# Kernel tuning notes

Hardware: AMD Instinct MI355X
Metric: run time of the kernel (lower is better)

Reference implementation:

```python
import jax, jax.numpy as jnp
import numpy as np
from jax import lax

N, B, C = 8192, 4, 16
H1, H2 = 64, 128
R = 0.7
K = 64  # max_num_neighbors


def setup_inputs() -> dict:
    key = jax.random.key(0)
    k1, k2, k3, k4, k5, k6 = jax.random.split(key, 6)
    x = jax.random.normal(k1, (N, C), dtype=jnp.float32)
    pos = jax.random.normal(k2, (N, 3), dtype=jnp.float32)
    batch = jnp.repeat(jnp.arange(B, dtype=jnp.int32), N // B)  # sorted segment ids
    # PointConv local MLP: Lin(C+3 -> H1), ReLU, Lin(H1 -> H2), ReLU
    W1 = jax.random.normal(k3, (C + 3, H1), dtype=jnp.float32) * np.sqrt(2.0 / (C + 3)).astype(np.float32)
    b1 = jnp.zeros((H1,), dtype=jnp.float32)
    W2 = jax.random.normal(k4, (H1, H2), dtype=jnp.float32) * np.sqrt(2.0 / H1).astype(np.float32)
    b2 = jnp.zeros((H2,), dtype=jnp.float32)
    return {"x": x, "pos": pos, "batch": batch, "W1": W1, "b1": b1, "W2": W2, "b2": b2}


def reference(x, pos, batch, W1, b1, W2, b2):
    # radius ball query: for every point (idx = arange(N), so all points are
    # centroids) take up to K neighbors within radius R in the same cloud.
    sq = jnp.sum(pos * pos, axis=-1)                       # [N]
    d2 = sq[:, None] + sq[None, :] - 2.0 * (pos @ pos.T)   # [N, N] squared dists
    valid = (d2 <= R * R) & (batch[:, None] == batch[None, :])
    score = jnp.where(valid, -d2, -jnp.inf)
    vals, idx = lax.top_k(score, K)                        # K nearest within ball
    mask = vals > -jnp.inf                                 # [N, K] real-neighbor mask

    # PointConv message: MLP(concat(x_j, pos_j - pos_i)), then max-aggregate.
    x_j = x[idx]                                           # [N, K, C]
    rel = pos[idx] - pos[:, None, :]                       # [N, K, 3]
    h = jnp.concatenate([x_j, rel], axis=-1)               # [N, K, C+3]
    h = jax.nn.relu(h @ W1 + b1)
    h = jax.nn.relu(h @ W2 + b2)                           # [N, K, H2]
    h = jnp.where(mask[..., None], h, -jnp.inf)
    out = jnp.max(h, axis=1)                               # self edge (d2=0) always valid
    return out, pos, batch
```

## Files before the change

kernel.cpp:

```cpp
#include <hip/hip_runtime.h>
#include <hip/hip_bf16.h>
#include <float.h>
#include <stdint.h>

#define NPTS 8192
#define SEG  2048
#define CF   16
#define HID1 64
#define HID2 128
#define KMAX 64
#define R2   0.49f
#define CAP  384
#define NCH  6

typedef unsigned long long ULL;
typedef short bf16x8 __attribute__((ext_vector_type(8)));
typedef float f32x4  __attribute__((ext_vector_type(4)));

__device__ __forceinline__ uint32_t f2ord(float f) {
    uint32_t u = __float_as_uint(f);
    return (u & 0x80000000u) ? ~u : (u | 0x80000000u);
}

__device__ __forceinline__ short f2bf(float f) {
    __hip_bfloat16 h = __float2bfloat16(f);
    union { __hip_bfloat16 b; short s; } u; u.b = h;
    return u.s;
}

__global__ __launch_bounds__(256) void prep_kernel(
    const float* __restrict__ x, const float* __restrict__ pos,
    const int* __restrict__ batch,
    const float* __restrict__ W1, const float* __restrict__ b1,
    const float* __restrict__ W2,
    float* __restrict__ A, float* __restrict__ C,
    float4* __restrict__ pos4, unsigned short* __restrict__ W2T,
    float* __restrict__ out)
{
    const int t = blockIdx.x * 256 + threadIdx.x;
    const int i = t >> 6, k = t & 63;

    const float px = pos[3 * i + 0], py = pos[3 * i + 1], pz = pos[3 * i + 2];
    float c = __fmul_rn(px, W1[16 * HID1 + k]);
    c = fmaf(py, W1[17 * HID1 + k], c);
    c = fmaf(pz, W1[18 * HID1 + k], c);

    float a = b1[k];
    #pragma unroll
    for (int cc = 0; cc < CF; ++cc)
        a = fmaf(x[i * CF + cc], W1[cc * HID1 + k], a);
    a += c;

    A[t] = a;
    C[t] = c;

    if (t < HID1 * HID2) {
        const int cc = t >> 6, kk = t & 63;
        W2T[t] = (unsigned short)f2bf(W2[kk * HID2 + cc]);
    }

    if (k == 0) {
        const float sq = __fadd_rn(__fadd_rn(__fmul_rn(px, px), __fmul_rn(py, py)),
                                   __fmul_rn(pz, pz));
        pos4[i] = make_float4(px, py, pz, sq);
    }
    if (k < 3) out[NPTS * HID2 + 3 * i + k] = pos[3 * i + k];
    if (k == 3) out[NPTS * HID2 + NPTS * 3 + i] = (float)batch[i];
}

__global__ __launch_bounds__(64, 3) void pointconv_kernel(
    const int* __restrict__ batch,
    const unsigned short* __restrict__ W2T, const float* __restrict__ b2,
    const float* __restrict__ A, const float* __restrict__ C,
    const float4* __restrict__ pos4, float* __restrict__ out)
{
    __shared__ ULL s_key[2][CAP];
    __shared__ int s_nbr[2][KMAX];

    const int l  = threadIdx.x;
    const int i0 = blockIdx.x * 2;

    const float4 cw0 = pos4[i0], cw1 = pos4[i0 + 1];
    const int seg0 = batch[i0] * SEG;
    const ULL lmask = (1ull << l) - 1ull;

    int cnt0 = 0, cnt1 = 0;
    #pragma unroll 4
    for (int it = 0; it < SEG / 64; ++it) {
        const int j = seg0 + it * 64 + l;
        const float4 pj = pos4[j];
        const float dot0 = fmaf(cw0.z, pj.z, fmaf(cw0.y, pj.y, __fmul_rn(cw0.x, pj.x)));
        const float d20  = __fsub_rn(__fadd_rn(cw0.w, pj.w), __fmul_rn(2.0f, dot0));
        const float dot1 = fmaf(cw1.z, pj.z, fmaf(cw1.y, pj.y, __fmul_rn(cw1.x, pj.x)));
        const float d21  = __fsub_rn(__fadd_rn(cw1.w, pj.w), __fmul_rn(2.0f, dot1));
        const bool h0 = (d20 <= R2), h1 = (d21 <= R2);
        const ULL m0 = __ballot(h0), m1 = __ballot(h1);
        if (h0) {
            const int p = cnt0 + __popcll(m0 & lmask);
            if (p < CAP) s_key[0][p] = ((ULL)f2ord(d20) << 32) | (unsigned)j;
        }
        cnt0 += __popcll(m0);
        if (h1) {
            const int p = cnt1 + __popcll(m1 & lmask);
            if (p < CAP) s_key[1][p] = ((ULL)f2ord(d21) << 32) | (unsigned)j;
        }
        cnt1 += __popcll(m1);
    }
    if (cnt0 > CAP) cnt0 = CAP;
    if (cnt1 > CAP) cnt1 = CAP;
    const bool nd0 = cnt0 > KMAX, nd1 = cnt1 > KMAX;

    uint32_t eo0[NCH], ej0[NCH], eo1[NCH], ej1[NCH];
    if (!nd0) {
        if (l < KMAX) s_nbr[0][l] = (l < cnt0) ? (int)(s_key[0][l] & 0xffffffffu) : i0;
    } else {
        #pragma unroll
        for (int g = 0; g < NCH; ++g) {
            eo0[g] = 0xffffffffu; ej0[g] = 0xffffffffu;
            if (64 * g < cnt0) {
                const int e = l + 64 * g;
                if (e < cnt0) {
                    const ULL kk = s_key[0][e];
                    eo0[g] = (uint32_t)(kk >> 32);
                    ej0[g] = (uint32_t)(kk & 0xffffffffu);
                }
            }
        }
    }
    if (!nd1) {
        if (l < KMAX) s_nbr[1][l] = (l < cnt1) ? (int)(s_key[1][l] & 0xffffffffu) : i0 + 1;
    } else {
        #pragma unroll
        for (int g = 0; g < NCH; ++g) {
            eo1[g] = 0xffffffffu; ej1[g] = 0xffffffffu;
            if (64 * g < cnt1) {
                const int e = l + 64 * g;
                if (e < cnt1) {
                    const ULL kk = s_key[1][e];
                    eo1[g] = (uint32_t)(kk >> 32);
                    ej1[g] = (uint32_t)(kk & 0xffffffffu);
                }
            }
        }
    }

    if (nd0 || nd1) {
        const uint32_t ORDR2 = 0x80000000u | __float_as_uint(R2);
        uint32_t lo0 = 0u, hi0 = nd0 ? ORDR2 : 0u;
        uint32_t lo1 = 0u, hi1 = nd1 ? ORDR2 : 0u;
        while ((lo0 < hi0) | (lo1 < hi1)) {
            if (lo0 < hi0) {
                const uint32_t mid = lo0 + ((hi0 - lo0) >> 1);
                int c = 0;
                #pragma unroll
                for (int g = 0; g < NCH; ++g)
                    if (64 * g < cnt0) c += __popcll(__ballot(eo0[g] <= mid));
                if (c >= KMAX) hi0 = mid; else lo0 = mid + 1;
            }
            if (lo1 < hi1) {
                const uint32_t mid = lo1 + ((hi1 - lo1) >> 1);
                int c = 0;
                #pragma unroll
                for (int g = 0; g < NCH; ++g)
                    if (64 * g < cnt1) c += __popcll(__ballot(eo1[g] <= mid));
                if (c >= KMAX) hi1 = mid; else lo1 = mid + 1;
            }
        }
        const uint32_t T0 = lo0, T1 = lo1;

        int cLT0 = 0, cLE0 = 0, cLT1 = 0, cLE1 = 0;
        if (nd0) {
            #pragma unroll
            for (int g = 0; g < NCH; ++g) {
                cLT0 += __popcll(__ballot(eo0[g] < T0));
                cLE0 += __popcll(__ballot(eo0[g] <= T0));
            }
        }
        if (nd1) {
            #pragma unroll
            for (int g = 0; g < NCH; ++g) {
                cLT1 += __popcll(__ballot(eo1[g] < T1));
                cLE1 += __popcll(__ballot(eo1[g] <= T1));
            }
        }

        uint32_t J0 = 0xffffffffu, J1 = 0xffffffffu;
        const bool tb0 = nd0 && (cLE0 > KMAX), tb1 = nd1 && (cLE1 > KMAX);
        if (tb0 | tb1) {
            uint32_t jlo0 = 0u, jhi0 = tb0 ? (NPTS - 1) : 0u;
            uint32_t jlo1 = 0u, jhi1 = tb1 ? (NPTS - 1) : 0u;
            const int need0 = KMAX - cLT0, need1 = KMAX - cLT1;
            while ((jlo0 < jhi0) | (jlo1 < jhi1)) {
                if (jlo0 < jhi0) {
                    const uint32_t jmid = jlo0 + ((jhi0 - jlo0) >> 1);
                    int c = 0;
                    #pragma unroll
                    for (int g = 0; g < NCH; ++g)
                        if (64 * g < cnt0) c += __popcll(__ballot(eo0[g] == T0 && ej0[g] <= jmid));
                    if (c >= need0) jhi0 = jmid; else jlo0 = jmid + 1;
                }
                if (jlo1 < jhi1) {
                    const uint32_t jmid = jlo1 + ((jhi1 - jlo1) >> 1);
                    int c = 0;
                    #pragma unroll
                    for (int g = 0; g < NCH; ++g)
                        if (64 * g < cnt1) c += __popcll(__ballot(eo1[g] == T1 && ej1[g] <= jmid));
                    if (c >= need1) jhi1 = jmid; else jlo1 = jmid + 1;
                }
            }
            if (tb0) J0 = jlo0;
            if (tb1) J1 = jlo1;
        }

        if (nd0) {
            int sb = 0;
            #pragma unroll
            for (int g = 0; g < NCH; ++g) {
                if (64 * g < cnt0) {
                    const bool take = (eo0[g] < T0) || ((eo0[g] == T0) && (ej0[g] <= J0));
                    const ULL mk = __ballot(take);
                    if (take) s_nbr[0][sb + __popcll(mk & lmask)] = (int)ej0[g];
                    sb += __popcll(mk);
                }
            }
        }
        if (nd1) {
            int sb = 0;
            #pragma unroll
            for (int g = 0; g < NCH; ++g) {
                if (64 * g < cnt1) {
                    const bool take = (eo1[g] < T1) || ((eo1[g] == T1) && (ej1[g] <= J1));
                    const ULL mk = __ballot(take);
                    if (take) s_nbr[1][sb + __popcll(mk & lmask)] = (int)ej1[g];
                    sb += __popcll(mk);
                }
            }
        }
    }

    const int r = l & 15, q = l >> 4;
    const int mm[2] = { cnt0 < KMAX ? cnt0 : KMAX, cnt1 < KMAX ? cnt1 : KMAX };

    bf16x8 af[2][4][2];
    #pragma unroll
    for (int ci = 0; ci < 2; ++ci) {
        const int iw = i0 + ci;
        float cv[2][8];
        {
            const float4* Cv = (const float4*)(C + (size_t)iw * HID1);
            #pragma unroll
            for (int kc = 0; kc < 2; ++kc) {
                const float4 c0 = Cv[kc * 8 + q * 2], c1 = Cv[kc * 8 + q * 2 + 1];
                cv[kc][0] = c0.x; cv[kc][1] = c0.y; cv[kc][2] = c0.z; cv[kc][3] = c0.w;
                cv[kc][4] = c1.x; cv[kc][5] = c1.y; cv[kc][6] = c1.z; cv[kc][7] = c1.w;
            }
        }
        #pragma unroll
        for (int t = 0; t < 4; ++t) {
            const int row = t * 16 + r;
            const int j = s_nbr[ci][row];
            const float4* Aj = (const float4*)(A + (size_t)j * HID1);
            #pragma unroll
            for (int kc = 0; kc < 2; ++kc) {
                const float4 a0 = Aj[kc * 8 + q * 2], a1 = Aj[kc * 8 + q * 2 + 1];
                bf16x8 v;
                v[0] = f2bf(fmaxf(a0.x - cv[kc][0], 0.0f));
                v[1] = f2bf(fmaxf(a0.y - cv[kc][1], 0.0f));
                v[2] = f2bf(fmaxf(a0.z - cv[kc][2], 0.0f));
                v[3] = f2bf(fmaxf(a0.w - cv[kc][3], 0.0f));
                v[4] = f2bf(fmaxf(a1.x - cv[kc][4], 0.0f));
                v[5] = f2bf(fmaxf(a1.y - cv[kc][5], 0.0f));
                v[6] = f2bf(fmaxf(a1.z - cv[kc][6], 0.0f));
                v[7] = f2bf(fmaxf(a1.w - cv[kc][7], 0.0f));
                af[ci][t][kc] = v;
            }
        }
    }

    #pragma unroll
    for (int cb = 0; cb < 8; ++cb) {
        f32x4 acc[2][4];
        #pragma unroll
        for (int ci = 0; ci < 2; ++ci)
            #pragma unroll
            for (int t = 0; t < 4; ++t) acc[ci][t] = (f32x4){0.f, 0.f, 0.f, 0.f};

        #pragma unroll
        for (int kc = 0; kc < 2; ++kc) {
            const bf16x8 bf =
                *(const bf16x8*)&W2T[(cb * 16 + r) * HID1 + kc * 32 + q * 8];
            #pragma unroll
            for (int ci = 0; ci < 2; ++ci)
                #pragma unroll
                for (int t = 0; t < 4; ++t)
                    acc[ci][t] = __builtin_amdgcn_mfma_f32_16x16x32_bf16(
                        af[ci][t][kc], bf, acc[ci][t], 0, 0, 0);
        }

        const int c = cb * 16 + r;
        #pragma unroll
        for (int ci = 0; ci < 2; ++ci) {
            float v = -FLT_MAX;
            #pragma unroll
            for (int t = 0; t < 4; ++t) {
                const int nb = t * 16 + q * 4;
                #pragma unroll
                for (int reg = 0; reg < 4; ++reg)
                    if (nb + reg < mm[ci]) v = fmaxf(v, acc[ci][t][reg]);
            }
            v = fmaxf(v, __shfl_xor(v, 16));
            v = fmaxf(v, __shfl_xor(v, 32));
            if (q == 0)
                out[(size_t)(i0 + ci) * HID2 + c] = fmaxf(v + b2[c], 0.0f);
        }
    }
}

extern "C" void kernel_launch(void* const* d_in, const int* in_sizes, int n_in,
                              void* d_out, int out_size, void* d_ws, size_t ws_size,
                              hipStream_t stream) {
    const float* x     = (const float*)d_in[0];
    const float* pos   = (const float*)d_in[1];
    const int*   batch = (const int*)d_in[2];
    const float* W1    = (const float*)d_in[3];
    const float* b1    = (const float*)d_in[4];
    const float* W2    = (const float*)d_in[5];
    const float* b2    = (const float*)d_in[6];
    float* out = (float*)d_out;

    float*  A    = (float*)d_ws;
    float*  C    = A + (size_t)NPTS * HID1;
    float4* P4   = (float4*)(C + (size_t)NPTS * HID1);
    unsigned short* W2T = (unsigned short*)(P4 + NPTS);

    hipLaunchKernelGGL(prep_kernel, dim3(NPTS * HID1 / 256), dim3(256), 0, stream,
                       x, pos, batch, W1, b1, W2, A, C, P4, W2T, out);
    hipLaunchKernelGGL(pointconv_kernel, dim3(NPTS / 2), dim3(64), 0, stream,
                       batch, W2T, b2, A, C, P4, out);
}
```

Before: 54.07 us.

## Process four centroids per block and share the neighbor scan across two waves

Each block now has two wavefronts and handles four centroids instead of two. Every neighbor position loaded in the scan is tested against all four centroids, and the segment is split between the two waves, so position traffic per centroid is halved. Candidate compaction now uses shared-memory atomic counters instead of wave ballots and prefix popcounts, which adds a block barrier. Each wave then runs selection and the MFMA stage for its two centroids. LDS atomics contend when many lanes hit the same centroid, and shared memory per block roughly doubles.

```diff
diff --git a/kernel.cpp b/kernel.cpp
--- a/kernel.cpp
+++ b/kernel.cpp
@@ -68,51 +68,57 @@
     if (k == 3) out[NPTS * HID2 + NPTS * 3 + i] = (float)batch[i];
 }
 
-__global__ __launch_bounds__(64, 3) void pointconv_kernel(
+__global__ __launch_bounds__(128, 3) void pointconv_kernel(
     const int* __restrict__ batch,
     const unsigned short* __restrict__ W2T, const float* __restrict__ b2,
     const float* __restrict__ A, const float* __restrict__ C,
     const float4* __restrict__ pos4, float* __restrict__ out)
 {
-    __shared__ ULL s_key[2][CAP];
-    __shared__ int s_nbr[2][KMAX];
-
-    const int l  = threadIdx.x;
-    const int i0 = blockIdx.x * 2;
-
-    const float4 cw0 = pos4[i0], cw1 = pos4[i0 + 1];
+    __shared__ ULL s_key[4][CAP];
+    __shared__ int s_nbr[4][KMAX];
+    __shared__ int s_cnt[4];
+
+    const int tid = threadIdx.x;
+    const int w   = tid >> 6, l = tid & 63;
+    const int i0  = blockIdx.x * 4;
+    const ULL lmask = (1ull << l) - 1ull;
+
+    if (tid < 4) s_cnt[tid] = 0;
+
+    float4 cw[4];
+    #pragma unroll
+    for (int ci = 0; ci < 4; ++ci) cw[ci] = pos4[i0 + ci];
     const int seg0 = batch[i0] * SEG;
-    const ULL lmask = (1ull << l) - 1ull;
-
-    int cnt0 = 0, cnt1 = 0;
-    #pragma unroll 4
-    for (int it = 0; it < SEG / 64; ++it) {
-        const int j = seg0 + it * 64 + l;
+    __syncthreads();
+
+    const int base = seg0 + w * (SEG / 2);
+    #pragma unroll 2
+    for (int it = 0; it < SEG / 128; ++it) {
+        const int j = base + it * 64 + l;
         const float4 pj = pos4[j];
-        const float dot0 = fmaf(cw0.z, pj.z, fmaf(cw0.y, pj.y, __fmul_rn(cw0.x, pj.x)));
-        const float d20  = __fsub_rn(__fadd_rn(cw0.w, pj.w), __fmul_rn(2.0f, dot0));
-        const float dot1 = fmaf(cw1.z, pj.z, fmaf(cw1.y, pj.y, __fmul_rn(cw1.x, pj.x)));
-        const float d21  = __fsub_rn(__fadd_rn(cw1.w, pj.w), __fmul_rn(2.0f, dot1));
-        const bool h0 = (d20 <= R2), h1 = (d21 <= R2);
-        const ULL m0 = __ballot(h0), m1 = __ballot(h1);
-        if (h0) {
-            const int p = cnt0 + __popcll(m0 & lmask);
-            if (p < CAP) s_key[0][p] = ((ULL)f2ord(d20) << 32) | (unsigned)j;
-        }
-        cnt0 += __popcll(m0);
-        if (h1) {
-            const int p = cnt1 + __popcll(m1 & lmask);
-            if (p < CAP) s_key[1][p] = ((ULL)f2ord(d21) << 32) | (unsigned)j;
-        }
-        cnt1 += __popcll(m1);
-    }
+        #pragma unroll
+        for (int ci = 0; ci < 4; ++ci) {
+            const float dot = fmaf(cw[ci].z, pj.z,
+                              fmaf(cw[ci].y, pj.y, __fmul_rn(cw[ci].x, pj.x)));
+            const float d2  = __fsub_rn(__fadd_rn(cw[ci].w, pj.w), __fmul_rn(2.0f, dot));
+            if (d2 <= R2) {
+                const int p = atomicAdd(&s_cnt[ci], 1);
+                if (p < CAP)
+                    s_key[ci][p] = ((ULL)f2ord(d2) << 32) | (unsigned)j;
+            }
+        }
+    }
+    __syncthreads();
+
+    const int c0i = 2 * w, c1i = 2 * w + 1;
+    int cnt0 = s_cnt[c0i], cnt1 = s_cnt[c1i];
     if (cnt0 > CAP) cnt0 = CAP;
     if (cnt1 > CAP) cnt1 = CAP;
     const bool nd0 = cnt0 > KMAX, nd1 = cnt1 > KMAX;
 
     uint32_t eo0[NCH], ej0[NCH], eo1[NCH], ej1[NCH];
     if (!nd0) {
-        if (l < KMAX) s_nbr[0][l] = (l < cnt0) ? (int)(s_key[0][l] & 0xffffffffu) : i0;
+        if (l < KMAX) s_nbr[c0i][l] = (l < cnt0) ? (int)(s_key[c0i][l] & 0xffffffffu) : i0 + c0i;
     } else {
         #pragma unroll
         for (int g = 0; g < NCH; ++g) {
@@ -120,7 +126,7 @@
             if (64 * g < cnt0) {
                 const int e = l + 64 * g;
                 if (e < cnt0) {
-                    const ULL kk = s_key[0][e];
+                    const ULL kk = s_key[c0i][e];
                     eo0[g] = (uint32_t)(kk >> 32);
                     ej0[g] = (uint32_t)(kk & 0xffffffffu);
                 }
@@ -128,7 +134,7 @@
         }
     }
     if (!nd1) {
-        if (l < KMAX) s_nbr[1][l] = (l < cnt1) ? (int)(s_key[1][l] & 0xffffffffu) : i0 + 1;
+        if (l < KMAX) s_nbr[c1i][l] = (l < cnt1) ? (int)(s_key[c1i][l] & 0xffffffffu) : i0 + c1i;
     } else {
         #pragma unroll
         for (int g = 0; g < NCH; ++g) {
@@ -136,7 +142,7 @@
             if (64 * g < cnt1) {
                 const int e = l + 64 * g;
                 if (e < cnt1) {
-                    const ULL kk = s_key[1][e];
+                    const ULL kk = s_key[c1i][e];
                     eo1[g] = (uint32_t)(kk >> 32);
                     ej1[g] = (uint32_t)(kk & 0xffffffffu);
                 }
@@ -219,7 +225,7 @@
                 if (64 * g < cnt0) {
                     const bool take = (eo0[g] < T0) || ((eo0[g] == T0) && (ej0[g] <= J0));
                     const ULL mk = __ballot(take);
-                    if (take) s_nbr[0][sb + __popcll(mk & lmask)] = (int)ej0[g];
+                    if (take) s_nbr[c0i][sb + __popcll(mk & lmask)] = (int)ej0[g];
                     sb += __popcll(mk);
                 }
             }
@@ -231,7 +237,7 @@
                 if (64 * g < cnt1) {
                     const bool take = (eo1[g] < T1) || ((eo1[g] == T1) && (ej1[g] <= J1));
                     const ULL mk = __ballot(take);
-                    if (take) s_nbr[1][sb + __popcll(mk & lmask)] = (int)ej1[g];
+                    if (take) s_nbr[c1i][sb + __popcll(mk & lmask)] = (int)ej1[g];
                     sb += __popcll(mk);
                 }
             }
@@ -243,7 +249,8 @@
 
     bf16x8 af[2][4][2];
     #pragma unroll
-    for (int ci = 0; ci < 2; ++ci) {
+    for (int cip = 0; cip < 2; ++cip) {
+        const int ci = 2 * w + cip;
         const int iw = i0 + ci;
         float cv[2][8];
         {
@@ -272,7 +279,7 @@
                 v[5] = f2bf(fmaxf(a1.y - cv[kc][5], 0.0f));
                 v[6] = f2bf(fmaxf(a1.z - cv[kc][6], 0.0f));
                 v[7] = f2bf(fmaxf(a1.w - cv[kc][7], 0.0f));
-                af[ci][t][kc] = v;
+                af[cip][t][kc] = v;
             }
         }
     }
@@ -281,37 +288,37 @@
     for (int cb = 0; cb < 8; ++cb) {
         f32x4 acc[2][4];
         #pragma unroll
-        for (int ci = 0; ci < 2; ++ci)
-            #pragma unroll
-            for (int t = 0; t < 4; ++t) acc[ci][t] = (f32x4){0.f, 0.f, 0.f, 0.f};
+        for (int cip = 0; cip < 2; ++cip)
+            #pragma unroll
+            for (int t = 0; t < 4; ++t) acc[cip][t] = (f32x4){0.f, 0.f, 0.f, 0.f};
 
         #pragma unroll
         for (int kc = 0; kc < 2; ++kc) {
             const bf16x8 bf =
                 *(const bf16x8*)&W2T[(cb * 16 + r) * HID1 + kc * 32 + q * 8];
             #pragma unroll
-            for (int ci = 0; ci < 2; ++ci)
+            for (int cip = 0; cip < 2; ++cip)
                 #pragma unroll
                 for (int t = 0; t < 4; ++t)
-                    acc[ci][t] = __builtin_amdgcn_mfma_f32_16x16x32_bf16(
-                        af[ci][t][kc], bf, acc[ci][t], 0, 0, 0);
+                    acc[cip][t] = __builtin_amdgcn_mfma_f32_16x16x32_bf16(
+                        af[cip][t][kc], bf, acc[cip][t], 0, 0, 0);
         }
 
         const int c = cb * 16 + r;
         #pragma unroll
-        for (int ci = 0; ci < 2; ++ci) {
+        for (int cip = 0; cip < 2; ++cip) {
             float v = -FLT_MAX;
             #pragma unroll
             for (int t = 0; t < 4; ++t) {
                 const int nb = t * 16 + q * 4;
                 #pragma unroll
                 for (int reg = 0; reg < 4; ++reg)
-                    if (nb + reg < mm[ci]) v = fmaxf(v, acc[ci][t][reg]);
+                    if (nb + reg < mm[cip]) v = fmaxf(v, acc[cip][t][reg]);
             }
             v = fmaxf(v, __shfl_xor(v, 16));
             v = fmaxf(v, __shfl_xor(v, 32));
             if (q == 0)
-                out[(size_t)(i0 + ci) * HID2 + c] = fmaxf(v + b2[c], 0.0f);
+                out[(size_t)(i0 + 2 * w + cip) * HID2 + c] = fmaxf(v + b2[c], 0.0f);
         }
     }
 }
@@ -335,6 +342,6 @@
 
     hipLaunchKernelGGL(prep_kernel, dim3(NPTS * HID1 / 256), dim3(256), 0, stream,
                        x, pos, batch, W1, b1, W2, A, C, P4, W2T, out);
-    hipLaunchKernelGGL(pointconv_kernel, dim3(NPTS / 2), dim3(64), 0, stream,
+    hipLaunchKernelGGL(pointconv_kernel, dim3(NPTS / 4), dim3(128), 0, stream,
                        batch, W2T, b2, A, C, P4, out);
 }
```

After: 71.92 us. +33.0%, slower.

## Split fused pointconv kernel into separate neighbor-select and MFMA kernels

Applied to the files above, without the earlier changes.

Splits the single kernel into a ball-query/top-K selection kernel, which writes neighbor indices and counts to global workspace, and a separate MFMA MLP kernel that reads them back. The aim is to let each phase run at higher occupancy (launch bounds raised to 6 and 4 waves) instead of carrying the register and LDS pressure of both phases. In exchange it adds a kernel launch and a global write and read of the N×K neighbor index array.

```diff
diff --git a/kernel.cpp b/kernel.cpp
--- a/kernel.cpp
+++ b/kernel.cpp
@@ -68,14 +68,11 @@
     if (k == 3) out[NPTS * HID2 + NPTS * 3 + i] = (float)batch[i];
 }
 
-__global__ __launch_bounds__(64, 3) void pointconv_kernel(
-    const int* __restrict__ batch,
-    const unsigned short* __restrict__ W2T, const float* __restrict__ b2,
-    const float* __restrict__ A, const float* __restrict__ C,
-    const float4* __restrict__ pos4, float* __restrict__ out)
+__global__ __launch_bounds__(64, 6) void select_kernel(
+    const int* __restrict__ batch, const float4* __restrict__ pos4,
+    int* __restrict__ nbr, int* __restrict__ mcnt)
 {
     __shared__ ULL s_key[2][CAP];
-    __shared__ int s_nbr[2][KMAX];
 
     const int l  = threadIdx.x;
     const int i0 = blockIdx.x * 2;
@@ -110,9 +107,15 @@
     if (cnt1 > CAP) cnt1 = CAP;
     const bool nd0 = cnt0 > KMAX, nd1 = cnt1 > KMAX;
 
+    if (l == 0) {
+        mcnt[i0]     = cnt0 < KMAX ? cnt0 : KMAX;
+        mcnt[i0 + 1] = cnt1 < KMAX ? cnt1 : KMAX;
+    }
+
     uint32_t eo0[NCH], ej0[NCH], eo1[NCH], ej1[NCH];
     if (!nd0) {
-        if (l < KMAX) s_nbr[0][l] = (l < cnt0) ? (int)(s_key[0][l] & 0xffffffffu) : i0;
+        if (l < KMAX)
+            nbr[(size_t)i0 * KMAX + l] = (l < cnt0) ? (int)(s_key[0][l] & 0xffffffffu) : i0;
     } else {
         #pragma unroll
         for (int g = 0; g < NCH; ++g) {
@@ -128,7 +131,8 @@
         }
     }
     if (!nd1) {
-        if (l < KMAX) s_nbr[1][l] = (l < cnt1) ? (int)(s_key[1][l] & 0xffffffffu) : i0 + 1;
+        if (l < KMAX)
+            nbr[(size_t)(i0 + 1) * KMAX + l] = (l < cnt1) ? (int)(s_key[1][l] & 0xffffffffu) : i0 + 1;
     } else {
         #pragma unroll
         for (int g = 0; g < NCH; ++g) {
@@ -219,7 +223,7 @@
                 if (64 * g < cnt0) {
                     const bool take = (eo0[g] < T0) || ((eo0[g] == T0) && (ej0[g] <= J0));
                     const ULL mk = __ballot(take);
-                    if (take) s_nbr[0][sb + __popcll(mk & lmask)] = (int)ej0[g];
+                    if (take) nbr[(size_t)i0 * KMAX + sb + __popcll(mk & lmask)] = (int)ej0[g];
                     sb += __popcll(mk);
                 }
             }
@@ -231,15 +235,25 @@
                 if (64 * g < cnt1) {
                     const bool take = (eo1[g] < T1) || ((eo1[g] == T1) && (ej1[g] <= J1));
                     const ULL mk = __ballot(take);
-                    if (take) s_nbr[1][sb + __popcll(mk & lmask)] = (int)ej1[g];
+                    if (take) nbr[(size_t)(i0 + 1) * KMAX + sb + __popcll(mk & lmask)] = (int)ej1[g];
                     sb += __popcll(mk);
                 }
             }
         }
     }
-
+}
+
+__global__ __launch_bounds__(64, 4) void mfma_kernel(
+    const unsigned short* __restrict__ W2T, const float* __restrict__ b2,
+    const float* __restrict__ A, const float* __restrict__ C,
+    const int* __restrict__ nbr, const int* __restrict__ mcnt,
+    float* __restrict__ out)
+{
+    const int l  = threadIdx.x;
+    const int i0 = blockIdx.x * 2;
     const int r = l & 15, q = l >> 4;
-    const int mm[2] = { cnt0 < KMAX ? cnt0 : KMAX, cnt1 < KMAX ? cnt1 : KMAX };
+
+    const int mm[2] = { mcnt[i0], mcnt[i0 + 1] };
 
     bf16x8 af[2][4][2];
     #pragma unroll
@@ -258,7 +272,7 @@
         #pragma unroll
         for (int t = 0; t < 4; ++t) {
             const int row = t * 16 + r;
-            const int j = s_nbr[ci][row];
+            const int j = nbr[(size_t)iw * KMAX + row];
             const float4* Aj = (const float4*)(A + (size_t)j * HID1);
             #pragma unroll
             for (int kc = 0; kc < 2; ++kc) {
@@ -332,9 +346,13 @@
     float*  C    = A + (size_t)NPTS * HID1;
     float4* P4   = (float4*)(C + (size_t)NPTS * HID1);
     unsigned short* W2T = (unsigned short*)(P4 + NPTS);
+    int* nbr  = (int*)(W2T + HID1 * HID2);
+    int* mcnt = nbr + (size_t)NPTS * KMAX;
 
     hipLaunchKernelGGL(prep_kernel, dim3(NPTS * HID1 / 256), dim3(256), 0, stream,
                        x, pos, batch, W1, b1, W2, A, C, P4, W2T, out);
-    hipLaunchKernelGGL(pointconv_kernel, dim3(NPTS / 2), dim3(64), 0, stream,
-                       batch, W2T, b2, A, C, P4, out);
-}
+    hipLaunchKernelGGL(select_kernel, dim3(NPTS / 2), dim3(64), 0, stream,
+                       batch, P4, nbr, mcnt);
+    hipLaunchKernelGGL(mfma_kernel, dim3(NPTS / 2), dim3(64), 0, stream,
+                       W2T, b2, A, C, nbr, mcnt, out);
+}
```

Measured after the change: 65.79 us. 1.22x slower.
